# Kernel tuning notes

Hardware: AMD Instinct MI355X
Metric: run time of the kernel (lower is better)

The kernel has to match this reference:

```python
import jax, jax.numpy as jnp
import numpy as np

N_NODES = 100000
N_EDGES = 1600000
HIDDEN = 128
NUM_FILTERS = 128
NUM_GAUSSIANS = 50
CUTOFF = 10.0
BOX = 5.0  # positions in [0,5]^3 so all pairwise distances < cutoff


def shifted_softplus(x):
    return jax.nn.softplus(x) - jnp.log(2.0)


def setup_inputs() -> dict:
    key = jax.random.key(0)
    ks = jax.random.split(key, 12)
    h = jax.random.normal(ks[0], (N_NODES, HIDDEN), jnp.float32)
    pos = jax.random.uniform(ks[1], (N_NODES, 3), jnp.float32) * BOX
    edge_index = jax.random.randint(ks[2], (2, N_EDGES), 0, N_NODES, jnp.int32)
    def lin(k, fan_in, fan_out):
        s = 1.0 / np.sqrt(fan_in)
        return jax.random.uniform(k, (fan_in, fan_out), jnp.float32, -s, s)
    return {
        "h": h,
        "pos": pos,
        "edge_index": edge_index,
        # CFConv filter network: Linear(NG, NF) -> ssp -> Linear(NF, NF)
        "mlp_w1": lin(ks[3], NUM_GAUSSIANS, NUM_FILTERS),
        "mlp_b1": jnp.zeros((NUM_FILTERS,), jnp.float32),
        "mlp_w2": lin(ks[4], NUM_FILTERS, NUM_FILTERS),
        "mlp_b2": jnp.zeros((NUM_FILTERS,), jnp.float32),
        # CFConv lin1 (no bias), lin2
        "lin1_w": lin(ks[5], HIDDEN, NUM_FILTERS),
        "lin2_w": lin(ks[6], NUM_FILTERS, HIDDEN),
        "lin2_b": jnp.zeros((HIDDEN,), jnp.float32),
        # InteractionBlock output linear
        "lin_w": lin(ks[7], HIDDEN, HIDDEN),
        "lin_b": jnp.zeros((HIDDEN,), jnp.float32),
    }


def reference(h, pos, edge_index, mlp_w1, mlp_b1, mlp_w2, mlp_b2,
              lin1_w, lin2_w, lin2_b, lin_w, lin_b):
    row, col = edge_index[0], edge_index[1]
    # edge distances (radius_graph neighbor list precomputed in setup_inputs)
    d = jnp.linalg.norm(pos[row] - pos[col], axis=-1)  # [E]
    # Gaussian smearing
    offset = jnp.linspace(0.0, CUTOFF, NUM_GAUSSIANS)
    coeff = -0.5 / (offset[1] - offset[0]) ** 2
    edge_attr = jnp.exp(coeff * (d[:, None] - offset[None, :]) ** 2)  # [E, NG]
    # CFConv: cosine cutoff * filter MLP
    C = 0.5 * (jnp.cos(d * jnp.pi / CUTOFF) + 1.0)  # [E]
    W = shifted_softplus(edge_attr @ mlp_w1 + mlp_b1) @ mlp_w2 + mlp_b2
    W = W * C[:, None]  # [E, NF]
    x = h @ lin1_w  # [N, NF]
    msgs = x[col] * W  # gather source feats, modulate by filter
    agg = jax.ops.segment_sum(msgs, row, num_segments=h.shape[0])  # scatter-add
    x = agg @ lin2_w + lin2_b
    # InteractionBlock tail: act -> linear
    x = shifted_softplus(x)
    x = x @ lin_w + lin_b
    return x
```

## Files before the change

kernel.cpp:

```cpp
#include <hip/hip_runtime.h>
#include <hip/hip_fp16.h>
#include <math.h>

constexpr int N_NODES = 100000;
constexpr int N_EDGES = 1600000;
constexpr int H       = 128;
constexpr int NG      = 50;
constexpr int EPT     = 32;
constexpr int NT      = N_EDGES / EPT;
constexpr int EBLK    = 2560;
constexpr int NBINS   = 98 * 1024;
constexpr int NODEB   = N_NODES / 32;

typedef _Float16 f16x8 __attribute__((ext_vector_type(8)));
typedef _Float16 f16x2 __attribute__((ext_vector_type(2)));
typedef float    f32x4 __attribute__((ext_vector_type(4)));

__device__ __forceinline__ float ssp_fast(float v) {
    return fmaxf(v, 0.0f) + __logf(1.0f + __expf(-fabsf(v))) - 0.69314718056f;
}

__device__ __forceinline__ void stage_tile_fp16(
    const float* __restrict__ src, _Float16* lds, int tid)
{
    const int row = tid >> 3;
    const int c0  = (tid & 7) * 16;
    const float* s = src + row * H + c0;
    #pragma unroll
    for (int half = 0; half < 2; ++half) {
        float4 f0 = *reinterpret_cast<const float4*>(s + half * 8);
        float4 f1 = *reinterpret_cast<const float4*>(s + half * 8 + 4);
        f16x8 v;
        v[0] = (_Float16)f0.x; v[1] = (_Float16)f0.y;
        v[2] = (_Float16)f0.z; v[3] = (_Float16)f0.w;
        v[4] = (_Float16)f1.x; v[5] = (_Float16)f1.y;
        v[6] = (_Float16)f1.z; v[7] = (_Float16)f1.w;
        unsigned off = (unsigned)(row * H + c0 + half * 8) * 2u;
        off ^= (unsigned)((row & 7) << 4);
        *reinterpret_cast<f16x8*>(reinterpret_cast<char*>(lds) + off) = v;
    }
}

__global__ __launch_bounds__(256) void prep0_kernel(
    const float* __restrict__ h, const float* __restrict__ w,
    __half* __restrict__ x, int* __restrict__ bins, float* __restrict__ agg)
{
    __shared__ alignas(16) _Float16 a_lds[32 * H];

    const int tid  = threadIdx.x;
    const int gtid = blockIdx.x * 256 + tid;
    const int gsz  = NODEB * 256;

    for (int i = gtid; i < NBINS; i += gsz) bins[i] = 0;
    {
        float4 z = {0.0f, 0.0f, 0.0f, 0.0f};
        float4* agg4 = reinterpret_cast<float4*>(agg);
        for (int i = gtid; i < N_NODES * H / 4; i += gsz) agg4[i] = z;
    }

    const int wv  = tid >> 6;
    const int l   = tid & 63;
    const int lhi = l >> 4;
    const int llo = l & 15;

    f16x8 bf[2][4];
    #pragma unroll
    for (int nf = 0; nf < 2; ++nf) {
        const int n = wv * 32 + nf * 16 + llo;
        #pragma unroll
        for (int ks = 0; ks < 4; ++ks)
            #pragma unroll
            for (int i = 0; i < 8; ++i)
                bf[nf][ks][i] = (_Float16)w[(ks * 32 + lhi * 8 + i) * H + n];
    }

    stage_tile_fp16(h + (size_t)blockIdx.x * 32 * H, a_lds, tid);
    __syncthreads();

    const f32x4 zero4 = {0.0f, 0.0f, 0.0f, 0.0f};
    f32x4 c[2][2];
    #pragma unroll
    for (int m = 0; m < 2; ++m)
        #pragma unroll
        for (int nf = 0; nf < 2; ++nf) c[m][nf] = zero4;

    #pragma unroll
    for (int msub = 0; msub < 2; ++msub) {
        const int rowa = msub * 16 + llo;
        #pragma unroll
        for (int ks = 0; ks < 4; ++ks) {
            unsigned off = (unsigned)(rowa * H) * 2u + (unsigned)(ks * 64 + lhi * 16);
            off ^= (unsigned)((rowa & 7) << 4);
            const f16x8 a = *reinterpret_cast<const f16x8*>(
                reinterpret_cast<const char*>(a_lds) + off);
            #pragma unroll
            for (int nf = 0; nf < 2; ++nf)
                c[msub][nf] = __builtin_amdgcn_mfma_f32_16x16x32_f16(
                    a, bf[nf][ks], c[msub][nf], 0, 0, 0);
        }
    }

    #pragma unroll
    for (int msub = 0; msub < 2; ++msub)
        #pragma unroll
        for (int nf = 0; nf < 2; ++nf)
            #pragma unroll
            for (int j = 0; j < 4; ++j) {
                const int node = blockIdx.x * 32 + msub * 16 + lhi * 4 + j;
                const int filt = wv * 32 + nf * 16 + llo;
                x[(size_t)node * H + filt] = __float2half(c[msub][nf][j]);
            }
}

__global__ __launch_bounds__(256) void hist_kernel(
    const int* __restrict__ ei, int* __restrict__ bins)
{
    const int e = blockIdx.x * 256 + threadIdx.x;
    if (e < N_EDGES) atomicAdd(&bins[ei[e]], 1);
}

__global__ __launch_bounds__(1024) void scanA_kernel(
    int* __restrict__ bins, int* __restrict__ bsum)
{
    __shared__ int ts[1024];
    const int i = blockIdx.x * 1024 + threadIdx.x;
    const int v = bins[i];
    ts[threadIdx.x] = v;
    __syncthreads();
    for (int d = 1; d < 1024; d <<= 1) {
        int t = (threadIdx.x >= d) ? ts[threadIdx.x - d] : 0;
        __syncthreads();
        ts[threadIdx.x] += t;
        __syncthreads();
    }
    bins[i] = ts[threadIdx.x] - v;
    if (threadIdx.x == 1023) bsum[blockIdx.x] = ts[1023];
}

__global__ __launch_bounds__(256) void scatter_kernel(
    const int* __restrict__ ei, const float* __restrict__ pos,
    int* __restrict__ bins, const int* __restrict__ bsum,
    int4* __restrict__ meta)
{
    __shared__ int pre[128];
    const int tid = threadIdx.x;
    int myv = 0;
    if (tid < 128) {
        myv = (tid < 98) ? bsum[tid] : 0;
        pre[tid] = myv;
    }
    __syncthreads();
    for (int d = 1; d < 128; d <<= 1) {
        int t = (tid < 128 && tid >= d) ? pre[tid - d] : 0;
        __syncthreads();
        if (tid < 128) pre[tid] += t;
        __syncthreads();
    }
    if (tid < 128) pre[tid] -= myv;
    __syncthreads();

    const int e = blockIdx.x * 256 + tid;
    if (e < N_EDGES) {
        const int r = ei[e];
        const int c = ei[N_EDGES + e];
        const int p = atomicAdd(&bins[r], 1) + pre[r >> 10];
        const float dx = pos[3 * r + 0] - pos[3 * c + 0];
        const float dy = pos[3 * r + 1] - pos[3 * c + 1];
        const float dz = pos[3 * r + 2] - pos[3 * c + 2];
        const float d  = sqrtf(dx * dx + dy * dy + dz * dz);
        const float cc = 0.5f * cosf(d * 0.31415926535897931f) + 0.5f;
        meta[p] = make_int4(r, __float_as_int(cc), c, __float_as_int(d));
    }
}

__global__ __launch_bounds__(256) void edge_kernel(
    const int4* __restrict__ meta, const __half* __restrict__ x,
    const float* __restrict__ w1, const float* __restrict__ b1,
    const float* __restrict__ w2, const float* __restrict__ b2,
    float* __restrict__ agg)
{
    __shared__ alignas(16) _Float16 t_lds[EPT * H];
    __shared__ alignas(16) _Float16 attr_lds[EPT * 64];

    const int tid = threadIdx.x;
    const int w   = tid >> 6;
    const int l   = tid & 63;
    const int lhi = l >> 4;
    const int llo = l & 15;

    constexpr float GSTEP = 10.0f / 49.0f;
    constexpr float GINV  = 4.9f;
    constexpr float GCOEF = -12.005f;

    f16x8 b1f[2][2];
    #pragma unroll
    for (int nf = 0; nf < 2; ++nf) {
        const int n = w * 32 + nf * 16 + llo;
        #pragma unroll
        for (int ks = 0; ks < 2; ++ks) {
            #pragma unroll
            for (int i = 0; i < 8; ++i) {
                const int k = ks * 32 + lhi * 8 + i;
                b1f[nf][ks][i] = (k < NG) ? (_Float16)w1[k * H + n] : (_Float16)0.0f;
            }
        }
    }
    f16x8 b2f[2][4];
    #pragma unroll
    for (int nf = 0; nf < 2; ++nf) {
        const int n = w * 32 + nf * 16 + llo;
        #pragma unroll
        for (int ks = 0; ks < 4; ++ks) {
            #pragma unroll
            for (int i = 0; i < 8; ++i) {
                const int k = ks * 32 + lhi * 8 + i;
                b2f[nf][ks][i] = (_Float16)w2[k * H + n];
            }
        }
    }
    const float b1v[2] = { b1[w * 32 + llo], b1[w * 32 + 16 + llo] };
    const float b2v[2] = { b2[w * 32 + llo], b2[w * 32 + 16 + llo] };

    const f32x4 zero4 = {0.0f, 0.0f, 0.0f, 0.0f};
    const f16x8 zf16  = {(_Float16)0, (_Float16)0, (_Float16)0, (_Float16)0,
                         (_Float16)0, (_Float16)0, (_Float16)0, (_Float16)0};

    for (int t = blockIdx.x; t < NT; t += gridDim.x) {
        const int4* mt = meta + (size_t)t * EPT;

        *reinterpret_cast<f16x8*>(
            reinterpret_cast<char*>(attr_lds) + tid * 16) = zf16;
        __syncthreads();

        {
            const int ae = tid >> 3;
            const int p  = tid & 7;
            const float d = __int_as_float(
                reinterpret_cast<const int*>(mt + ae)[3]);
            int g0 = (int)(d * GINV + 0.5f) - 7;
            g0 &= ~1;
            g0 = max(0, min(48, g0));
            const int g = g0 + 2 * p;
            const float df0 = d - (float)g * GSTEP;
            const float df1 = d - (float)(g + 1) * GSTEP;
            f16x2 v;
            v[0] = (_Float16)__expf(GCOEF * df0 * df0);
            v[1] = (_Float16)__expf(GCOEF * df1 * df1);
            unsigned off = (unsigned)(ae * 128 + g * 2);
            off ^= (unsigned)((ae & 7) << 4);
            *reinterpret_cast<f16x2*>(
                reinterpret_cast<char*>(attr_lds) + off) = v;
        }
        __syncthreads();

        float xv[2][4][2];
        #pragma unroll
        for (int msub = 0; msub < 2; ++msub)
            #pragma unroll
            for (int j = 0; j < 4; ++j) {
                const int edge = msub * 16 + lhi * 4 + j;
                const int col  = reinterpret_cast<const int*>(mt + edge)[2];
                const int cbase = col * H + w * 32 + llo;
                xv[msub][j][0] = __half2float(x[cbase]);
                xv[msub][j][1] = __half2float(x[cbase + 16]);
            }

        f32x4 c1[2][2];
        #pragma unroll
        for (int m = 0; m < 2; ++m)
            #pragma unroll
            for (int nf = 0; nf < 2; ++nf) c1[m][nf] = zero4;

        #pragma unroll
        for (int msub = 0; msub < 2; ++msub) {
            const int ea = msub * 16 + llo;
            #pragma unroll
            for (int ks = 0; ks < 2; ++ks) {
                unsigned off = (unsigned)(ea * 128 + ks * 64 + lhi * 16);
                off ^= (unsigned)((ea & 7) << 4);
                const f16x8 a1 = *reinterpret_cast<const f16x8*>(
                    reinterpret_cast<const char*>(attr_lds) + off);
                #pragma unroll
                for (int nf = 0; nf < 2; ++nf)
                    c1[msub][nf] = __builtin_amdgcn_mfma_f32_16x16x32_f16(
                        a1, b1f[nf][ks], c1[msub][nf], 0, 0, 0);
            }
        }

        #pragma unroll
        for (int msub = 0; msub < 2; ++msub)
            #pragma unroll
            for (int nf = 0; nf < 2; ++nf)
                #pragma unroll
                for (int j = 0; j < 4; ++j) {
                    const int edge = msub * 16 + lhi * 4 + j;
                    const int filt = w * 32 + nf * 16 + llo;
                    const float tv = ssp_fast(c1[msub][nf][j] + b1v[nf]);
                    unsigned off = (unsigned)(edge * H + filt) * 2u;
                    off ^= (unsigned)((edge & 7) << 4);
                    *reinterpret_cast<_Float16*>(
                        reinterpret_cast<char*>(t_lds) + off) = (_Float16)tv;
                }

        __syncthreads();

        int2 rcA[2][4];
        #pragma unroll
        for (int msub = 0; msub < 2; ++msub)
            #pragma unroll
            for (int j = 0; j < 4; ++j)
                rcA[msub][j] = *reinterpret_cast<const int2*>(
                    mt + msub * 16 + lhi * 4 + j);

        f32x4 c2[2][2];
        #pragma unroll
        for (int m = 0; m < 2; ++m)
            #pragma unroll
            for (int nf = 0; nf < 2; ++nf) c2[m][nf] = zero4;

        #pragma unroll
        for (int ks = 0; ks < 4; ++ks) {
            f16x8 a2[2];
            #pragma unroll
            for (int msub = 0; msub < 2; ++msub) {
                const int edge = msub * 16 + llo;
                unsigned off = (unsigned)(edge * H) * 2u
                             + (unsigned)(ks * 64 + lhi * 16);
                off ^= (unsigned)((edge & 7) << 4);
                a2[msub] = *reinterpret_cast<const f16x8*>(
                    reinterpret_cast<const char*>(t_lds) + off);
            }
            #pragma unroll
            for (int msub = 0; msub < 2; ++msub)
                #pragma unroll
                for (int nf = 0; nf < 2; ++nf)
                    c2[msub][nf] = __builtin_amdgcn_mfma_f32_16x16x32_f16(
                        a2[msub], b2f[nf][ks], c2[msub][nf], 0, 0, 0);
        }

        #pragma unroll
        for (int msub = 0; msub < 2; ++msub) {
            int rr[4]; float cce[4];
            #pragma unroll
            for (int j = 0; j < 4; ++j) {
                rr[j]  = rcA[msub][j].x;
                cce[j] = __int_as_float(rcA[msub][j].y);
            }
            const bool bB1 = rr[1] != rr[0];
            const bool bB2 = rr[2] != rr[1];
            const bool bB3 = rr[3] != rr[2];
            const bool closed = bB1 | bB2 | bB3;
            const int  prev_t = __shfl_up(rr[3], 16);
            const int  next_h = __shfl_down(rr[0], 16);
            const bool mrg  = (lhi > 0) && (rr[0] == prev_t);
            const bool sing = !closed;
            const bool issue_tail = (lhi == 3) || (next_h != rr[3]);

            float v0[4], v1[4];
            #pragma unroll
            for (int j = 0; j < 4; ++j) {
                v0[j] = (c2[msub][0][j] + b2v[0]) * cce[j] * xv[msub][j][0];
                v1[j] = (c2[msub][1][j] + b2v[1]) * cce[j] * xv[msub][j][1];
            }
            const int fc0 = w * 32 + llo;
            const int fc1 = fc0 + 16;

            float h0 = v0[0], h1 = v1[0];
            if (!bB1) { h0 += v0[1]; h1 += v1[1];
                if (!bB2) { h0 += v0[2]; h1 += v1[2];
                    if (!bB3) { h0 += v0[3]; h1 += v1[3]; } } }
            float cs0 = v0[3], cs1 = v1[3];
            if (!bB3) { cs0 += v0[2]; cs1 += v1[2];
                if (!bB2) { cs0 += v0[1]; cs1 += v1[1];
                    if (!bB1) { cs0 += v0[0]; cs1 += v1[0]; } } }

            if (bB1 && bB2) { atomicAdd(&agg[rr[1] * H + fc0], v0[1]);
                              atomicAdd(&agg[rr[1] * H + fc1], v1[1]); }
            if (bB2 && bB3) { atomicAdd(&agg[rr[2] * H + fc0], v0[2]);
                              atomicAdd(&agg[rr[2] * H + fc1], v1[2]); }
            if (bB1 && !bB2 && bB3) {
                atomicAdd(&agg[rr[1] * H + fc0], v0[1] + v0[2]);
                atomicAdd(&agg[rr[1] * H + fc1], v1[1] + v1[2]);
            }

            bool f = !(sing && mrg);
            {
                float p0 = __shfl_up(cs0, 16), p1 = __shfl_up(cs1, 16);
                int   pf = __shfl_up((int)f, 16);
                if (lhi >= 1 && !f) { cs0 += p0; cs1 += p1; f = (bool)pf; }
            }
            {
                float p0 = __shfl_up(cs0, 32), p1 = __shfl_up(cs1, 32);
                int   pf = __shfl_up((int)f, 32);
                if (lhi >= 2 && !f) { cs0 += p0; cs1 += p1; f = (bool)pf; }
            }
            const float car0 = __shfl_up(cs0, 16);
            const float car1 = __shfl_up(cs1, 16);

            if (closed) {
                atomicAdd(&agg[rr[0] * H + fc0], h0 + (mrg ? car0 : 0.0f));
                atomicAdd(&agg[rr[0] * H + fc1], h1 + (mrg ? car1 : 0.0f));
            }
            if (issue_tail) {
                atomicAdd(&agg[rr[3] * H + fc0], cs0);
                atomicAdd(&agg[rr[3] * H + fc1], cs1);
            }
        }
    }
}

__global__ __launch_bounds__(256) void final_kernel(
    const float* __restrict__ agg,
    const float* __restrict__ w2l, const float* __restrict__ b2l,
    const float* __restrict__ wl,  const float* __restrict__ bl,
    float* __restrict__ out)
{
    __shared__ alignas(16) _Float16 a_lds[32 * H];
    __shared__ alignas(16) _Float16 t_lds[32 * H];

    const int tid = threadIdx.x;
    const int wv  = tid >> 6;
    const int l   = tid & 63;
    const int lhi = l >> 4;
    const int llo = l & 15;

    f16x8 b1f[2][4], b2f[2][4];
    #pragma unroll
    for (int nf = 0; nf < 2; ++nf) {
        const int n = wv * 32 + nf * 16 + llo;
        #pragma unroll
        for (int ks = 0; ks < 4; ++ks)
            #pragma unroll
            for (int i = 0; i < 8; ++i) {
                const int k = ks * 32 + lhi * 8 + i;
                b1f[nf][ks][i] = (_Float16)w2l[k * H + n];
                b2f[nf][ks][i] = (_Float16)wl[k * H + n];
            }
    }
    const float b2v[2] = { b2l[wv * 32 + llo], b2l[wv * 32 + 16 + llo] };
    const float bv[2]  = { bl[wv * 32 + llo],  bl[wv * 32 + 16 + llo]  };

    stage_tile_fp16(agg + (size_t)blockIdx.x * 32 * H, a_lds, tid);
    __syncthreads();

    const f32x4 zero4 = {0.0f, 0.0f, 0.0f, 0.0f};
    f32x4 c1[2][2];
    #pragma unroll
    for (int m = 0; m < 2; ++m)
        #pragma unroll
        for (int nf = 0; nf < 2; ++nf) c1[m][nf] = zero4;

    #pragma unroll
    for (int msub = 0; msub < 2; ++msub) {
        const int rowa = msub * 16 + llo;
        #pragma unroll
        for (int ks = 0; ks < 4; ++ks) {
            unsigned off = (unsigned)(rowa * H) * 2u + (unsigned)(ks * 64 + lhi * 16);
            off ^= (unsigned)((rowa & 7) << 4);
            const f16x8 a = *reinterpret_cast<const f16x8*>(
                reinterpret_cast<const char*>(a_lds) + off);
            #pragma unroll
            for (int nf = 0; nf < 2; ++nf)
                c1[msub][nf] = __builtin_amdgcn_mfma_f32_16x16x32_f16(
                    a, b1f[nf][ks], c1[msub][nf], 0, 0, 0);
        }
    }

    #pragma unroll
    for (int msub = 0; msub < 2; ++msub)
        #pragma unroll
        for (int nf = 0; nf < 2; ++nf)
            #pragma unroll
            for (int j = 0; j < 4; ++j) {
                const int rowc = msub * 16 + lhi * 4 + j;
                const int filt = wv * 32 + nf * 16 + llo;
                const float tv = ssp_fast(c1[msub][nf][j] + b2v[nf]);
                unsigned off = (unsigned)(rowc * H + filt) * 2u;
                off ^= (unsigned)((rowc & 7) << 4);
                *reinterpret_cast<_Float16*>(
                    reinterpret_cast<char*>(t_lds) + off) = (_Float16)tv;
            }

    __syncthreads();

    f32x4 c2[2][2];
    #pragma unroll
    for (int m = 0; m < 2; ++m)
        #pragma unroll
        for (int nf = 0; nf < 2; ++nf) c2[m][nf] = zero4;

    #pragma unroll
    for (int msub = 0; msub < 2; ++msub) {
        const int rowa = msub * 16 + llo;
        #pragma unroll
        for (int ks = 0; ks < 4; ++ks) {
            unsigned off = (unsigned)(rowa * H) * 2u + (unsigned)(ks * 64 + lhi * 16);
            off ^= (unsigned)((rowa & 7) << 4);
            const f16x8 a = *reinterpret_cast<const f16x8*>(
                reinterpret_cast<const char*>(t_lds) + off);
            #pragma unroll
            for (int nf = 0; nf < 2; ++nf)
                c2[msub][nf] = __builtin_amdgcn_mfma_f32_16x16x32_f16(
                    a, b2f[nf][ks], c2[msub][nf], 0, 0, 0);
        }
    }

    #pragma unroll
    for (int msub = 0; msub < 2; ++msub)
        #pragma unroll
        for (int nf = 0; nf < 2; ++nf)
            #pragma unroll
            for (int j = 0; j < 4; ++j) {
                const int node = blockIdx.x * 32 + msub * 16 + lhi * 4 + j;
                const int filt = wv * 32 + nf * 16 + llo;
                out[(size_t)node * H + filt] = c2[msub][nf][j] + bv[nf];
            }
}

extern "C" void kernel_launch(void* const* d_in, const int* in_sizes, int n_in,
                              void* d_out, int out_size, void* d_ws, size_t ws_size,
                              hipStream_t stream) {
    const float* h      = (const float*)d_in[0];
    const float* pos    = (const float*)d_in[1];
    const int*   ei     = (const int*)  d_in[2];
    const float* mlp_w1 = (const float*)d_in[3];
    const float* mlp_b1 = (const float*)d_in[4];
    const float* mlp_w2 = (const float*)d_in[5];
    const float* mlp_b2 = (const float*)d_in[6];
    const float* lin1_w = (const float*)d_in[7];
    const float* lin2_w = (const float*)d_in[8];
    const float* lin2_b = (const float*)d_in[9];
    const float* lin_w  = (const float*)d_in[10];
    const float* lin_b  = (const float*)d_in[11];

    float* out = (float*)d_out;
    char*  ws  = (char*)d_ws;
    float* agg  = (float*)ws;
    char*  p    = ws + (size_t)N_NODES * H * 4;
    int*   bins = (int*)p;
    int*   bsum = (int*)(p + (size_t)NBINS * 4);

    __half* x    = (__half*)d_out;
    int4*   meta = (int4*)((char*)d_out + (size_t)N_NODES * H * 2);

    prep0_kernel<<<NODEB, 256, 0, stream>>>(h, lin1_w, x, bins, agg);
    hist_kernel<<<(N_EDGES + 255) / 256, 256, 0, stream>>>(ei, bins);
    scanA_kernel<<<NBINS / 1024, 1024, 0, stream>>>(bins, bsum);
    scatter_kernel<<<(N_EDGES + 255) / 256, 256, 0, stream>>>(ei, pos, bins,
                                                              bsum, meta);
    edge_kernel<<<EBLK, 256, 0, stream>>>(meta, x, mlp_w1, mlp_b1,
                                          mlp_w2, mlp_b2, agg);
    final_kernel<<<NODEB, 256, 0, stream>>>(agg, lin2_w, lin2_b,
                                            lin_w, lin_b, out);
}
```

Baseline: 501.8 us.

## Fuse histogram into prep kernel, pack x as half2, fold biases into MFMA init

The edge-row histogram moves into the prep kernel as a grid-stride loop, and the bins are cleared with hipMemsetAsync instead of a separate kernel pass. x is stored interleaved as half2 so each gather in the edge kernel is one 4-byte load instead of two 2-byte loads. The edge kernel gets a minimum-occupancy launch bound, and the final kernel starts its MFMA accumulators at the bias values instead of adding the bias afterwards. This removes one kernel launch and some gather instructions. The bins must now be zero before prep0 runs, which the memset ensures, and the occupancy hint may force register spills.

```diff
diff --git a/kernel.cpp b/kernel.cpp
--- a/kernel.cpp
+++ b/kernel.cpp
@@ -42,8 +42,9 @@
 }
 
 __global__ __launch_bounds__(256) void prep0_kernel(
-    const float* __restrict__ h, const float* __restrict__ w,
-    __half* __restrict__ x, int* __restrict__ bins, float* __restrict__ agg)
+    const int* __restrict__ ei, const float* __restrict__ h,
+    const float* __restrict__ w, __half2* __restrict__ xp,
+    int* __restrict__ bins, float* __restrict__ agg)
 {
     __shared__ alignas(16) _Float16 a_lds[32 * H];
 
@@ -51,7 +52,6 @@
     const int gtid = blockIdx.x * 256 + tid;
     const int gsz  = NODEB * 256;
 
-    for (int i = gtid; i < NBINS; i += gsz) bins[i] = 0;
     {
         float4 z = {0.0f, 0.0f, 0.0f, 0.0f};
         float4* agg4 = reinterpret_cast<float4*>(agg);
@@ -103,20 +103,14 @@
     #pragma unroll
     for (int msub = 0; msub < 2; ++msub)
         #pragma unroll
-        for (int nf = 0; nf < 2; ++nf)
-            #pragma unroll
-            for (int j = 0; j < 4; ++j) {
-                const int node = blockIdx.x * 32 + msub * 16 + lhi * 4 + j;
-                const int filt = wv * 32 + nf * 16 + llo;
-                x[(size_t)node * H + filt] = __float2half(c[msub][nf][j]);
-            }
-}
-
-__global__ __launch_bounds__(256) void hist_kernel(
-    const int* __restrict__ ei, int* __restrict__ bins)
-{
-    const int e = blockIdx.x * 256 + threadIdx.x;
-    if (e < N_EDGES) atomicAdd(&bins[ei[e]], 1);
+        for (int j = 0; j < 4; ++j) {
+            const int node = blockIdx.x * 32 + msub * 16 + lhi * 4 + j;
+            xp[(size_t)node * 64 + wv * 16 + llo] =
+                __floats2half2_rn(c[msub][0][j], c[msub][1][j]);
+        }
+
+    for (int e = gtid; e < N_EDGES; e += gsz)
+        atomicAdd(&bins[ei[e]], 1);
 }
 
 __global__ __launch_bounds__(1024) void scanA_kernel(
@@ -173,8 +167,8 @@
     }
 }
 
-__global__ __launch_bounds__(256) void edge_kernel(
-    const int4* __restrict__ meta, const __half* __restrict__ x,
+__global__ __launch_bounds__(256, 4) void edge_kernel(
+    const int4* __restrict__ meta, const __half2* __restrict__ xp,
     const float* __restrict__ w1, const float* __restrict__ b1,
     const float* __restrict__ w2, const float* __restrict__ b2,
     float* __restrict__ agg)
@@ -260,9 +254,9 @@
             for (int j = 0; j < 4; ++j) {
                 const int edge = msub * 16 + lhi * 4 + j;
                 const int col  = reinterpret_cast<const int*>(mt + edge)[2];
-                const int cbase = col * H + w * 32 + llo;
-                xv[msub][j][0] = __half2float(x[cbase]);
-                xv[msub][j][1] = __half2float(x[cbase + 16]);
+                const float2 fv = __half22float2(xp[col * 64 + w * 16 + llo]);
+                xv[msub][j][0] = fv.x;
+                xv[msub][j][1] = fv.y;
             }
 
         f32x4 c1[2][2];
@@ -443,12 +437,14 @@
     stage_tile_fp16(agg + (size_t)blockIdx.x * 32 * H, a_lds, tid);
     __syncthreads();
 
-    const f32x4 zero4 = {0.0f, 0.0f, 0.0f, 0.0f};
     f32x4 c1[2][2];
     #pragma unroll
     for (int m = 0; m < 2; ++m)
         #pragma unroll
-        for (int nf = 0; nf < 2; ++nf) c1[m][nf] = zero4;
+        for (int nf = 0; nf < 2; ++nf) {
+            c1[m][nf][0] = b2v[nf]; c1[m][nf][1] = b2v[nf];
+            c1[m][nf][2] = b2v[nf]; c1[m][nf][3] = b2v[nf];
+        }
 
     #pragma unroll
     for (int msub = 0; msub < 2; ++msub) {
@@ -474,7 +470,7 @@
             for (int j = 0; j < 4; ++j) {
                 const int rowc = msub * 16 + lhi * 4 + j;
                 const int filt = wv * 32 + nf * 16 + llo;
-                const float tv = ssp_fast(c1[msub][nf][j] + b2v[nf]);
+                const float tv = ssp_fast(c1[msub][nf][j]);
                 unsigned off = (unsigned)(rowc * H + filt) * 2u;
                 off ^= (unsigned)((rowc & 7) << 4);
                 *reinterpret_cast<_Float16*>(
@@ -487,7 +483,10 @@
     #pragma unroll
     for (int m = 0; m < 2; ++m)
         #pragma unroll
-        for (int nf = 0; nf < 2; ++nf) c2[m][nf] = zero4;
+        for (int nf = 0; nf < 2; ++nf) {
+            c2[m][nf][0] = bv[nf]; c2[m][nf][1] = bv[nf];
+            c2[m][nf][2] = bv[nf]; c2[m][nf][3] = bv[nf];
+        }
 
     #pragma unroll
     for (int msub = 0; msub < 2; ++msub) {
@@ -513,7 +512,7 @@
             for (int j = 0; j < 4; ++j) {
                 const int node = blockIdx.x * 32 + msub * 16 + lhi * 4 + j;
                 const int filt = wv * 32 + nf * 16 + llo;
-                out[(size_t)node * H + filt] = c2[msub][nf][j] + bv[nf];
+                out[(size_t)node * H + filt] = c2[msub][nf][j];
             }
 }
 
@@ -540,15 +539,15 @@
     int*   bins = (int*)p;
     int*   bsum = (int*)(p + (size_t)NBINS * 4);
 
-    __half* x    = (__half*)d_out;
-    int4*   meta = (int4*)((char*)d_out + (size_t)N_NODES * H * 2);
-
-    prep0_kernel<<<NODEB, 256, 0, stream>>>(h, lin1_w, x, bins, agg);
-    hist_kernel<<<(N_EDGES + 255) / 256, 256, 0, stream>>>(ei, bins);
+    __half2* xp  = (__half2*)d_out;
+    int4*   meta = (int4*)((char*)d_out + (size_t)N_NODES * 64 * 4);
+
+    hipMemsetAsync(bins, 0, (size_t)NBINS * sizeof(int), stream);
+    prep0_kernel<<<NODEB, 256, 0, stream>>>(ei, h, lin1_w, xp, bins, agg);
     scanA_kernel<<<NBINS / 1024, 1024, 0, stream>>>(bins, bsum);
     scatter_kernel<<<(N_EDGES + 255) / 256, 256, 0, stream>>>(ei, pos, bins,
                                                               bsum, meta);
-    edge_kernel<<<EBLK, 256, 0, stream>>>(meta, x, mlp_w1, mlp_b1,
+    edge_kernel<<<EBLK, 256, 0, stream>>>(meta, xp, mlp_w1, mlp_b1,
                                           mlp_w2, mlp_b2, agg);
     final_kernel<<<NODEB, 256, 0, stream>>>(agg, lin2_w, lin2_b,
                                             lin_w, lin_b, out);
```

After: 829.1 us. 1.65x slower.
